# Kernel tuning notes

Hardware: AMD Instinct MI355X
Metric: run time of the kernel (lower is better)

## Reference

```python
import jax, jax.numpy as jnp
import numpy as np

B, H, W = 8, 512, 512
KSIZE = 11   # HVS Gaussian kernel size
SIGMA = 2.0
EPS = 1e-8


def _gauss_kernel():
    ax = jnp.arange(KSIZE, dtype=jnp.float32) - (KSIZE - 1) / 2.0
    g = jnp.exp(-(ax ** 2) / (2.0 * SIGMA ** 2))
    k = jnp.outer(g, g)
    return k / jnp.sum(k)


def _conv_same(x, k):
    # x: (B,1,H,W), k: (kh,kw) symmetric -> conv == correlation
    return jax.lax.conv_general_dilated(
        x, k[None, None, :, :], window_strides=(1, 1), padding='SAME',
        dimension_numbers=('NCHW', 'OIHW', 'NCHW'))


def setup_inputs() -> dict:
    key = jax.random.key(0)
    k1, k2, k3 = jax.random.split(key, 3)
    prob_map = jax.random.uniform(k1, (B, 1, H, W), dtype=jnp.float32,
                                  minval=0.01, maxval=0.99)
    c = jax.random.uniform(k2, (B, 1, H, W), dtype=jnp.float32)
    # binary halftone sampled per-pixel from prob_map
    h_sampled = (jax.random.uniform(k3, (B, 1, H, W)) < prob_map).astype(jnp.float32)
    return {"prob_map": prob_map, "c": c, "h_sampled": h_sampled}


def reference(prob_map, c, h_sampled):
    k = _gauss_kernel()
    # perceived error of the sampled halftone: e = G*h - c
    e = _conv_same(h_sampled, k) - c                     # (B,1,H,W)
    corr = _conv_same(e, k)                              # (G*e), G symmetric
    sum_k2 = jnp.sum(k * k)
    delta = 1.0 - 2.0 * h_sampled                        # flip change per pixel
    # reward_calc.compute_reward_with_flip, vectorized over all pixels:
    # E(flip at a) - E = 2*delta_a*(G*e)(a) + delta_a^2 * sum(G^2)
    reward = 2.0 * delta * corr + (delta ** 2) * sum_k2  # >0 means flip hurts
    log_prob = jnp.where(h_sampled > 0.5,
                         jnp.log(prob_map + EPS),
                         jnp.log(1.0 - prob_map + EPS))
    # local expected-gradient (REINFORCE) loss, averaged over batch
    loss = -jnp.sum(reward * log_prob) / prob_map.shape[0]
    return loss
```

## Files before the change

kernel.cpp:

```cpp
#include <hip/hip_runtime.h>

typedef float v2f __attribute__((ext_vector_type(2)));
typedef float v4f __attribute__((ext_vector_type(4)));

#define IMG 512
#define TS  32
#define TPB 2
#define NBLK 1024

#define A_STR  56
#define BT_STR 46
#define E_STR  44
#define CT_STR 34
#define C_STR  48

__device__ __forceinline__ v2f lo2(v4f v) { return __builtin_shufflevector(v, v, 0, 1); }
__device__ __forceinline__ v2f hi2(v4f v) { return __builtin_shufflevector(v, v, 2, 3); }

__device__ __forceinline__ v4f ldq(const float* __restrict__ hmap, size_t base,
                                   int x0, int y0, int idx) {
    int r = idx / 14, q = idx - r * 14;
    int gy = y0 - 10 + r, gx0 = x0 - 12 + 4 * q;
    v4f v = {0.f, 0.f, 0.f, 0.f};
    if ((unsigned)gy < IMG) {
        const float* hr = &hmap[base + ((size_t)gy << 9)];
        if (gx0 >= 0 && gx0 + 3 < IMG) {
            v = *(const v4f*)&hr[gx0];
        } else {
            if ((unsigned)(gx0 + 0) < IMG) v.x = hr[gx0 + 0];
            if ((unsigned)(gx0 + 1) < IMG) v.y = hr[gx0 + 1];
            if ((unsigned)(gx0 + 2) < IMG) v.z = hr[gx0 + 2];
            if ((unsigned)(gx0 + 3) < IMG) v.w = hr[gx0 + 3];
        }
    }
    return v;
}

__device__ __forceinline__ v4f ldc(const float* __restrict__ cmap, size_t base,
                                   int x0, int y0, int idx) {
    int r = idx / 12, q = idx - r * 12;
    int gy = y0 - 5 + r, gx0 = x0 - 8 + 4 * q;
    v4f v = {0.f, 0.f, 0.f, 0.f};
    if ((unsigned)gy < IMG) {
        const float* cr = &cmap[base + ((size_t)gy << 9)];
        if (gx0 >= 0 && gx0 + 3 < IMG) {
            v = *(const v4f*)&cr[gx0];
        } else {
            if ((unsigned)(gx0 + 0) < IMG) v.x = cr[gx0 + 0];
            if ((unsigned)(gx0 + 1) < IMG) v.y = cr[gx0 + 1];
            if ((unsigned)(gx0 + 2) < IMG) v.z = cr[gx0 + 2];
            if ((unsigned)(gx0 + 3) < IMG) v.w = cr[gx0 + 3];
        }
    }
    return v;
}

__global__ __launch_bounds__(256, 4) void marl_fused(
    const float* __restrict__ prob,
    const float* __restrict__ cmap,
    const float* __restrict__ hmap,
    float* __restrict__ out)
{
    __shared__ __align__(16) float Abuf[52 * A_STR];
    __shared__ __align__(16) float Bbuf[56 * BT_STR];
    __shared__ __align__(16) float Cbuf[42 * C_STR];
    __shared__ float red[4];

    const float W[11] = {0.00881223f, 0.02714358f, 0.06511405f, 0.12164908f,
                         0.17699840f, 0.20056540f, 0.17699840f, 0.12164908f,
                         0.06511405f, 0.02714358f, 0.00881223f};
    v2f wv[11];
#pragma unroll
    for (int i = 0; i < 11; ++i) wv[i] = (v2f){W[i], W[i]};
    float w2 = 0.f;
#pragma unroll
    for (int i = 0; i < 11; ++i) w2 += W[i] * W[i];
    const float sumk2 = w2 * w2;
    const v2f z = {0.f, 0.f};

    const int tid = threadIdx.x;
    const int wk  = (tid & 63) * 4 + (tid >> 6);
    const int i0 = tid, i1 = tid + 256, i2 = tid + 512;
    const int T0 = blockIdx.x * TPB;

    const int ox0 = 2 * (tid & 15), oy0e = 2 * (tid >> 4);

    v2f hv[TPB][2], pv[TPB][2];

    {
        const int b = T0 >> 8, r8 = T0 & 255;
        const int x0 = (r8 & 15) * TS, y0 = (r8 >> 4) * TS;
        const size_t base = (size_t)b << 18;
        v4f ha = ldq(hmap, base, x0, y0, i0);
        v4f hb = ldq(hmap, base, x0, y0, i1);
        v4f hc = (tid < 216) ? ldq(hmap, base, x0, y0, i2) : (v4f){0.f,0.f,0.f,0.f};
        v4f ca = ldc(cmap, base, x0, y0, i0);
        v4f cb = (tid < 248) ? ldc(cmap, base, x0, y0, i1) : (v4f){0.f,0.f,0.f,0.f};
#pragma unroll
        for (int h = 0; h < 2; ++h) {
            size_t rowb = base + ((size_t)(y0 + oy0e + h) << 9) + (x0 + ox0);
            hv[0][h] = *(const v2f*)&hmap[rowb];
            pv[0][h] = *(const v2f*)&prob[rowb];
        }
        { int r = i0 / 14, q = i0 - r * 14; *(v4f*)&Abuf[r * A_STR + 4 * q] = ha; }
        { int r = i1 / 14, q = i1 - r * 14; *(v4f*)&Abuf[r * A_STR + 4 * q] = hb; }
        if (tid < 216) { int r = i2 / 14, q = i2 - r * 14; *(v4f*)&Abuf[r * A_STR + 4 * q] = hc; }
        { int r = i0 / 12, q = i0 - r * 12; *(v4f*)&Cbuf[r * C_STR + 4 * q] = ca; }
        if (tid < 248) { int r = i1 / 12, q = i1 - r * 12; *(v4f*)&Cbuf[r * C_STR + 4 * q] = cb; }
    }
    __syncthreads();

    float partial = 0.f;
    v4f pfh0, pfh1, pfh2, pfc0, pfc1;

#pragma unroll
    for (int t = 0; t < TPB; ++t) {
        const int T = T0 + t;
        const int r8 = T & 255;
        const int x0 = (r8 & 15) * TS, y0 = (r8 >> 4) * TS;

        if (wk < 196) {
            int q = wk % 14, run = wk / 14;
            int by0 = 3 * run;
            v2f accLo[3] = {z, z, z}, accHi[3] = {z, z, z};
#pragma unroll
            for (int i = 0; i < 13; ++i) {
                v4f a = *(const v4f*)&Abuf[(by0 + i) * A_STR + 4 * q];
                v2f lo = lo2(a), hi = hi2(a);
#pragma unroll
                for (int r = 0; r < 3; ++r) {
                    int j = i - r;
                    if (j >= 0 && j < 11) { accLo[r] += wv[j] * lo; accHi[r] += wv[j] * hi; }
                }
            }
#pragma unroll
            for (int r = 0; r < 3; ++r) {
                int by = by0 + r;
                Bbuf[(4 * q + 0) * BT_STR + by] = accLo[r].x;
                Bbuf[(4 * q + 1) * BT_STR + by] = accLo[r].y;
                Bbuf[(4 * q + 2) * BT_STR + by] = accHi[r].x;
                Bbuf[(4 * q + 3) * BT_STR + by] = accHi[r].y;
            }
        }
        __syncthreads();

        if (wk < 231) {
            int eq = wk % 11, p = wk / 11;
            int ex0 = 4 * eq, ey0 = 2 * p;
            v2f acc[4] = {z, z, z, z};
#pragma unroll
            for (int i = 0; i < 14; ++i) {
                v2f bb = *(const v2f*)&Bbuf[(ex0 + 2 + i) * BT_STR + ey0];
#pragma unroll
                for (int c = 0; c < 4; ++c) {
                    int j = i - c;
                    if (j >= 0 && j < 11) acc[c] += wv[j] * bb;
                }
            }
#pragma unroll
            for (int c = 0; c < 4; ++c) {
                int ex = ex0 + c;
                if (ex < 42) {
                    int gx = x0 - 5 + ex;
                    bool xin = (unsigned)gx < IMG;
#pragma unroll
                    for (int h = 0; h < 2; ++h) {
                        int gy = y0 - 5 + ey0 + h;
                        float v = 0.f;
                        if (xin && (unsigned)gy < IMG)
                            v = acc[c][h] - Cbuf[(ey0 + h) * C_STR + ex + 3];
                        Abuf[(ey0 + h) * E_STR + ex] = v;
                    }
                }
            }
        }
        __syncthreads();

        if (t + 1 < TPB) {
            const int Tn = T + 1;
            const int nb = Tn >> 8, nr8 = Tn & 255;
            const int nx0 = (nr8 & 15) * TS, ny0 = (nr8 >> 4) * TS;
            const size_t nbase = (size_t)nb << 18;
            pfh0 = ldq(hmap, nbase, nx0, ny0, i0);
            pfh1 = ldq(hmap, nbase, nx0, ny0, i1);
            if (tid < 216) pfh2 = ldq(hmap, nbase, nx0, ny0, i2);
            pfc0 = ldc(cmap, nbase, nx0, ny0, i0);
            if (tid < 248) pfc1 = ldc(cmap, nbase, nx0, ny0, i1);
#pragma unroll
            for (int h = 0; h < 2; ++h) {
                size_t rowb = nbase + ((size_t)(ny0 + oy0e + h) << 9) + (nx0 + ox0);
                hv[t + 1][h] = *(const v2f*)&hmap[rowb];
                pv[t + 1][h] = *(const v2f*)&prob[rowb];
            }
        }
        if (wk < 176) {
            int eq = wk % 11, run = wk / 11;
            int ex0 = 4 * eq, oyb = 2 * run;
            v2f accLo[2] = {z, z}, accHi[2] = {z, z};
#pragma unroll
            for (int i = 0; i < 12; ++i) {
                v4f e = *(const v4f*)&Abuf[(oyb + i) * E_STR + ex0];
                v2f lo = lo2(e), hi = hi2(e);
#pragma unroll
                for (int r = 0; r < 2; ++r) {
                    int j = i - r;
                    if (j >= 0 && j < 11) { accLo[r] += wv[j] * lo; accHi[r] += wv[j] * hi; }
                }
            }
#pragma unroll
            for (int r = 0; r < 2; ++r) {
                int oy = oyb + r;
                Bbuf[(ex0 + 0) * CT_STR + oy] = accLo[r].x;
                Bbuf[(ex0 + 1) * CT_STR + oy] = accLo[r].y;
                if (ex0 + 2 < 42) {
                    Bbuf[(ex0 + 2) * CT_STR + oy] = accHi[r].x;
                    Bbuf[(ex0 + 3) * CT_STR + oy] = accHi[r].y;
                }
            }
        }
        __syncthreads();

        if (t + 1 < TPB) {
            { int r = i0 / 14, q = i0 - r * 14; *(v4f*)&Abuf[r * A_STR + 4 * q] = pfh0; }
            { int r = i1 / 14, q = i1 - r * 14; *(v4f*)&Abuf[r * A_STR + 4 * q] = pfh1; }
            if (tid < 216) { int r = i2 / 14, q = i2 - r * 14; *(v4f*)&Abuf[r * A_STR + 4 * q] = pfh2; }
            { int r = i0 / 12, q = i0 - r * 12; *(v4f*)&Cbuf[r * C_STR + 4 * q] = pfc0; }
            if (tid < 248) { int r = i1 / 12, q = i1 - r * 12; *(v4f*)&Cbuf[r * C_STR + 4 * q] = pfc1; }
        }
        {
            v2f acc[2] = {z, z};
#pragma unroll
            for (int i = 0; i < 12; ++i) {
                v2f ct = *(const v2f*)&Bbuf[(ox0 + i) * CT_STR + oy0e];
#pragma unroll
                for (int c = 0; c < 2; ++c) {
                    int j = i - c;
                    if (j >= 0 && j < 11) acc[c] += wv[j] * ct;
                }
            }
#pragma unroll
            for (int h = 0; h < 2; ++h) {
#pragma unroll
                for (int c = 0; c < 2; ++c) {
                    float h_ = hv[t][h][c], p_ = pv[t][h][c];
                    float logp = __logf(h_ > 0.5f ? p_ + 1e-8f : 1.f - p_ + 1e-8f);
                    float delta = 1.f - 2.f * h_;
                    partial += (2.f * delta * acc[c][h] + sumk2) * logp;
                }
            }
        }
        __syncthreads();
    }

#pragma unroll
    for (int off = 32; off > 0; off >>= 1)
        partial += __shfl_down(partial, off, 64);
    if ((tid & 63) == 0) red[tid >> 6] = partial;
    __syncthreads();
    if (tid == 0) {
        float s = red[0] + red[1] + red[2] + red[3];
        atomicAdd(out, s * -0.125f);
    }
}

extern "C" void kernel_launch(void* const* d_in, const int* in_sizes, int n_in,
                              void* d_out, int out_size, void* d_ws, size_t ws_size,
                              hipStream_t stream) {
    const float* prob = (const float*)d_in[0];
    const float* cmap = (const float*)d_in[1];
    const float* hmap = (const float*)d_in[2];
    float* out = (float*)d_out;

    hipMemsetAsync(out, 0, sizeof(float), stream);

    marl_fused<<<dim3(NBLK), dim3(256), 0, stream>>>(prob, cmap, hmap, out);
}
```

Measured before the change: 94.71 us.

## Use 32x16 tiles, one tile per block, and swizzle the error buffer in LDS

Replaces the two-tiles-per-block 32x32 scheme (with register prefetch of the next tile) by one 32x16 tile per block over 4096 blocks. Halo loads, work mappings and LDS strides are reworked to fit the smaller tile, and the error buffer gets an XOR swizzle to cut LDS bank conflicts. Launch bounds rise to 8 blocks per CU to raise occupancy. The cost is more halo overhead per output pixel, since the halo ratio is worse for shorter tiles, plus more idle threads in each stage and the loss of the cross-tile prefetch overlap.

```diff
diff --git a/kernel.cpp b/kernel.cpp
--- a/kernel.cpp
+++ b/kernel.cpp
@@ -4,15 +4,15 @@
 typedef float v4f __attribute__((ext_vector_type(4)));
 
 #define IMG 512
-#define TS  32
-#define TPB 2
-#define NBLK 1024
-
-#define A_STR  56
-#define BT_STR 46
-#define E_STR  44
-#define CT_STR 34
-#define C_STR  48
+#define TSX 32
+#define TSY 16
+#define NBLK 4096
+
+#define A_STR  60
+#define BT_STR 28
+#define E_STR  64
+#define CT_STR 18
+#define C_STR  49
 
 __device__ __forceinline__ v2f lo2(v4f v) { return __builtin_shufflevector(v, v, 0, 1); }
 __device__ __forceinline__ v2f hi2(v4f v) { return __builtin_shufflevector(v, v, 2, 3); }
@@ -55,15 +55,15 @@
     return v;
 }
 
-__global__ __launch_bounds__(256, 4) void marl_fused(
+__global__ __launch_bounds__(256, 8) void marl_fused(
     const float* __restrict__ prob,
     const float* __restrict__ cmap,
     const float* __restrict__ hmap,
     float* __restrict__ out)
 {
-    __shared__ __align__(16) float Abuf[52 * A_STR];
+    __shared__ __align__(16) float Abuf[36 * A_STR];
     __shared__ __align__(16) float Bbuf[56 * BT_STR];
-    __shared__ __align__(16) float Cbuf[42 * C_STR];
+    __shared__ __align__(16) float Cbuf[26 * C_STR];
     __shared__ float red[4];
 
     const float W[11] = {0.00881223f, 0.02714358f, 0.06511405f, 0.12164908f,
@@ -79,177 +79,148 @@
     const v2f z = {0.f, 0.f};
 
     const int tid = threadIdx.x;
-    const int wk  = (tid & 63) * 4 + (tid >> 6);
-    const int i0 = tid, i1 = tid + 256, i2 = tid + 512;
-    const int T0 = blockIdx.x * TPB;
-
-    const int ox0 = 2 * (tid & 15), oy0e = 2 * (tid >> 4);
-
-    v2f hv[TPB][2], pv[TPB][2];
-
+    const int T  = blockIdx.x;
+    const int b  = T >> 9, r9 = T & 511;
+    const int x0 = (r9 & 15) * TSX, y0 = (r9 >> 4) * TSY;
+    const size_t base = (size_t)b << 18;
+
+    const int ox0 = 2 * (tid >> 3), oy0e = 2 * (tid & 7);
+
+    v2f hv[2], pv[2];
     {
-        const int b = T0 >> 8, r8 = T0 & 255;
-        const int x0 = (r8 & 15) * TS, y0 = (r8 >> 4) * TS;
-        const size_t base = (size_t)b << 18;
-        v4f ha = ldq(hmap, base, x0, y0, i0);
-        v4f hb = ldq(hmap, base, x0, y0, i1);
-        v4f hc = (tid < 216) ? ldq(hmap, base, x0, y0, i2) : (v4f){0.f,0.f,0.f,0.f};
-        v4f ca = ldc(cmap, base, x0, y0, i0);
-        v4f cb = (tid < 248) ? ldc(cmap, base, x0, y0, i1) : (v4f){0.f,0.f,0.f,0.f};
-#pragma unroll
-        for (int h = 0; h < 2; ++h) {
-            size_t rowb = base + ((size_t)(y0 + oy0e + h) << 9) + (x0 + ox0);
-            hv[0][h] = *(const v2f*)&hmap[rowb];
-            pv[0][h] = *(const v2f*)&prob[rowb];
-        }
-        { int r = i0 / 14, q = i0 - r * 14; *(v4f*)&Abuf[r * A_STR + 4 * q] = ha; }
-        { int r = i1 / 14, q = i1 - r * 14; *(v4f*)&Abuf[r * A_STR + 4 * q] = hb; }
-        if (tid < 216) { int r = i2 / 14, q = i2 - r * 14; *(v4f*)&Abuf[r * A_STR + 4 * q] = hc; }
-        { int r = i0 / 12, q = i0 - r * 12; *(v4f*)&Cbuf[r * C_STR + 4 * q] = ca; }
-        if (tid < 248) { int r = i1 / 12, q = i1 - r * 12; *(v4f*)&Cbuf[r * C_STR + 4 * q] = cb; }
-    }
-    __syncthreads();
-
-    float partial = 0.f;
-    v4f pfh0, pfh1, pfh2, pfc0, pfc1;
-
-#pragma unroll
-    for (int t = 0; t < TPB; ++t) {
-        const int T = T0 + t;
-        const int r8 = T & 255;
-        const int x0 = (r8 & 15) * TS, y0 = (r8 >> 4) * TS;
-
-        if (wk < 196) {
-            int q = wk % 14, run = wk / 14;
-            int by0 = 3 * run;
-            v2f accLo[3] = {z, z, z}, accHi[3] = {z, z, z};
-#pragma unroll
-            for (int i = 0; i < 13; ++i) {
-                v4f a = *(const v4f*)&Abuf[(by0 + i) * A_STR + 4 * q];
-                v2f lo = lo2(a), hi = hi2(a);
-#pragma unroll
-                for (int r = 0; r < 3; ++r) {
-                    int j = i - r;
-                    if (j >= 0 && j < 11) { accLo[r] += wv[j] * lo; accHi[r] += wv[j] * hi; }
-                }
-            }
+        v4f ha = ldq(hmap, base, x0, y0, tid);
+        v4f hb = (tid < 248) ? ldq(hmap, base, x0, y0, tid + 256) : (v4f){0.f,0.f,0.f,0.f};
+        v4f ca = ldc(cmap, base, x0, y0, tid);
+        v4f cb = (tid < 56) ? ldc(cmap, base, x0, y0, tid + 256) : (v4f){0.f,0.f,0.f,0.f};
+        if (tid < 128) {
+#pragma unroll
+            for (int h = 0; h < 2; ++h) {
+                size_t rowb = base + ((size_t)(y0 + oy0e + h) << 9) + (x0 + ox0);
+                hv[h] = *(const v2f*)&hmap[rowb];
+                pv[h] = *(const v2f*)&prob[rowb];
+            }
+        }
+        { int r = tid / 14, q = tid - r * 14; *(v4f*)&Abuf[r * A_STR + 4 * q] = ha; }
+        if (tid < 248) { int i = tid + 256, r = i / 14, q = i - r * 14;
+                         *(v4f*)&Abuf[r * A_STR + 4 * q] = hb; }
+        { int r = tid / 12, q = tid - r * 12; float* d = &Cbuf[r * C_STR + 4 * q];
+          d[0] = ca.x; d[1] = ca.y; d[2] = ca.z; d[3] = ca.w; }
+        if (tid < 56) { int i = tid + 256, r = i / 12, q = i - r * 12;
+                        float* d = &Cbuf[r * C_STR + 4 * q];
+                        d[0] = cb.x; d[1] = cb.y; d[2] = cb.z; d[3] = cb.w; }
+    }
+    __syncthreads();
+
+    if (tid < 126) {
+        int q = tid / 9, run = tid - 9 * q;
+        int by0 = 3 * run;
+        v2f accLo[3] = {z, z, z}, accHi[3] = {z, z, z};
+#pragma unroll
+        for (int i = 0; i < 13; ++i) {
+            v4f a = *(const v4f*)&Abuf[(by0 + i) * A_STR + 4 * q];
+            v2f lo = lo2(a), hi = hi2(a);
 #pragma unroll
             for (int r = 0; r < 3; ++r) {
-                int by = by0 + r;
+                int j = i - r;
+                if (j >= 0 && j < 11) { accLo[r] += wv[j] * lo; accHi[r] += wv[j] * hi; }
+            }
+        }
+#pragma unroll
+        for (int r = 0; r < 3; ++r) {
+            int by = by0 + r;
+            if (by < 26) {
                 Bbuf[(4 * q + 0) * BT_STR + by] = accLo[r].x;
                 Bbuf[(4 * q + 1) * BT_STR + by] = accLo[r].y;
                 Bbuf[(4 * q + 2) * BT_STR + by] = accHi[r].x;
                 Bbuf[(4 * q + 3) * BT_STR + by] = accHi[r].y;
             }
         }
-        __syncthreads();
-
-        if (wk < 231) {
-            int eq = wk % 11, p = wk / 11;
-            int ex0 = 4 * eq, ey0 = 2 * p;
-            v2f acc[4] = {z, z, z, z};
-#pragma unroll
-            for (int i = 0; i < 14; ++i) {
-                v2f bb = *(const v2f*)&Bbuf[(ex0 + 2 + i) * BT_STR + ey0];
-#pragma unroll
-                for (int c = 0; c < 4; ++c) {
-                    int j = i - c;
-                    if (j >= 0 && j < 11) acc[c] += wv[j] * bb;
+    }
+    __syncthreads();
+
+    if (tid < 143) {
+        int eq = tid / 13, p = tid - 13 * eq;
+        int ex0 = 4 * eq, ey0 = 2 * p;
+        v2f acc[4] = {z, z, z, z};
+#pragma unroll
+        for (int i = 0; i < 14; ++i) {
+            v2f bb = *(const v2f*)&Bbuf[(ex0 + 2 + i) * BT_STR + ey0];
+#pragma unroll
+            for (int c = 0; c < 4; ++c) {
+                int j = i - c;
+                if (j >= 0 && j < 11) acc[c] += wv[j] * bb;
+            }
+        }
+        int swz = (p & 7) << 2;
+#pragma unroll
+        for (int c = 0; c < 4; ++c) {
+            int ex = ex0 + c;
+            if (ex < 42) {
+                int gx = x0 - 5 + ex;
+                bool xin = (unsigned)gx < IMG;
+#pragma unroll
+                for (int h = 0; h < 2; ++h) {
+                    int gy = y0 - 5 + ey0 + h;
+                    float v = 0.f;
+                    if (xin && (unsigned)gy < IMG)
+                        v = acc[c][h] - Cbuf[(ey0 + h) * C_STR + ex + 3];
+                    Abuf[(ey0 + h) * E_STR + (ex ^ swz)] = v;
                 }
             }
-#pragma unroll
-            for (int c = 0; c < 4; ++c) {
-                int ex = ex0 + c;
-                if (ex < 42) {
-                    int gx = x0 - 5 + ex;
-                    bool xin = (unsigned)gx < IMG;
-#pragma unroll
-                    for (int h = 0; h < 2; ++h) {
-                        int gy = y0 - 5 + ey0 + h;
-                        float v = 0.f;
-                        if (xin && (unsigned)gy < IMG)
-                            v = acc[c][h] - Cbuf[(ey0 + h) * C_STR + ex + 3];
-                        Abuf[(ey0 + h) * E_STR + ex] = v;
-                    }
-                }
-            }
-        }
-        __syncthreads();
-
-        if (t + 1 < TPB) {
-            const int Tn = T + 1;
-            const int nb = Tn >> 8, nr8 = Tn & 255;
-            const int nx0 = (nr8 & 15) * TS, ny0 = (nr8 >> 4) * TS;
-            const size_t nbase = (size_t)nb << 18;
-            pfh0 = ldq(hmap, nbase, nx0, ny0, i0);
-            pfh1 = ldq(hmap, nbase, nx0, ny0, i1);
-            if (tid < 216) pfh2 = ldq(hmap, nbase, nx0, ny0, i2);
-            pfc0 = ldc(cmap, nbase, nx0, ny0, i0);
-            if (tid < 248) pfc1 = ldc(cmap, nbase, nx0, ny0, i1);
-#pragma unroll
-            for (int h = 0; h < 2; ++h) {
-                size_t rowb = nbase + ((size_t)(ny0 + oy0e + h) << 9) + (nx0 + ox0);
-                hv[t + 1][h] = *(const v2f*)&hmap[rowb];
-                pv[t + 1][h] = *(const v2f*)&prob[rowb];
-            }
-        }
-        if (wk < 176) {
-            int eq = wk % 11, run = wk / 11;
-            int ex0 = 4 * eq, oyb = 2 * run;
-            v2f accLo[2] = {z, z}, accHi[2] = {z, z};
-#pragma unroll
-            for (int i = 0; i < 12; ++i) {
-                v4f e = *(const v4f*)&Abuf[(oyb + i) * E_STR + ex0];
-                v2f lo = lo2(e), hi = hi2(e);
-#pragma unroll
-                for (int r = 0; r < 2; ++r) {
-                    int j = i - r;
-                    if (j >= 0 && j < 11) { accLo[r] += wv[j] * lo; accHi[r] += wv[j] * hi; }
-                }
-            }
+        }
+    }
+    __syncthreads();
+
+    if (tid < 88) {
+        int eq = tid >> 3, run = tid & 7;
+        int ex0 = 4 * eq, oy0 = 2 * run;
+        v2f accLo[2] = {z, z}, accHi[2] = {z, z};
+#pragma unroll
+        for (int i = 0; i < 12; ++i) {
+            int row = oy0 + i;
+            v4f e = *(const v4f*)&Abuf[row * E_STR + (ex0 ^ (((row >> 1) & 7) << 2))];
+            v2f lo = lo2(e), hi = hi2(e);
 #pragma unroll
             for (int r = 0; r < 2; ++r) {
-                int oy = oyb + r;
-                Bbuf[(ex0 + 0) * CT_STR + oy] = accLo[r].x;
-                Bbuf[(ex0 + 1) * CT_STR + oy] = accLo[r].y;
-                if (ex0 + 2 < 42) {
-                    Bbuf[(ex0 + 2) * CT_STR + oy] = accHi[r].x;
-                    Bbuf[(ex0 + 3) * CT_STR + oy] = accHi[r].y;
-                }
-            }
-        }
-        __syncthreads();
-
-        if (t + 1 < TPB) {
-            { int r = i0 / 14, q = i0 - r * 14; *(v4f*)&Abuf[r * A_STR + 4 * q] = pfh0; }
-            { int r = i1 / 14, q = i1 - r * 14; *(v4f*)&Abuf[r * A_STR + 4 * q] = pfh1; }
-            if (tid < 216) { int r = i2 / 14, q = i2 - r * 14; *(v4f*)&Abuf[r * A_STR + 4 * q] = pfh2; }
-            { int r = i0 / 12, q = i0 - r * 12; *(v4f*)&Cbuf[r * C_STR + 4 * q] = pfc0; }
-            if (tid < 248) { int r = i1 / 12, q = i1 - r * 12; *(v4f*)&Cbuf[r * C_STR + 4 * q] = pfc1; }
-        }
-        {
-            v2f acc[2] = {z, z};
-#pragma unroll
-            for (int i = 0; i < 12; ++i) {
-                v2f ct = *(const v2f*)&Bbuf[(ox0 + i) * CT_STR + oy0e];
-#pragma unroll
-                for (int c = 0; c < 2; ++c) {
-                    int j = i - c;
-                    if (j >= 0 && j < 11) acc[c] += wv[j] * ct;
-                }
-            }
-#pragma unroll
-            for (int h = 0; h < 2; ++h) {
-#pragma unroll
-                for (int c = 0; c < 2; ++c) {
-                    float h_ = hv[t][h][c], p_ = pv[t][h][c];
-                    float logp = __logf(h_ > 0.5f ? p_ + 1e-8f : 1.f - p_ + 1e-8f);
-                    float delta = 1.f - 2.f * h_;
-                    partial += (2.f * delta * acc[c][h] + sumk2) * logp;
-                }
-            }
-        }
-        __syncthreads();
+                int j = i - r;
+                if (j >= 0 && j < 11) { accLo[r] += wv[j] * lo; accHi[r] += wv[j] * hi; }
+            }
+        }
+#pragma unroll
+        for (int r = 0; r < 2; ++r) {
+            int oy = oy0 + r;
+            Bbuf[(ex0 + 0) * CT_STR + oy] = accLo[r].x;
+            Bbuf[(ex0 + 1) * CT_STR + oy] = accLo[r].y;
+            if (ex0 + 2 < 42) {
+                Bbuf[(ex0 + 2) * CT_STR + oy] = accHi[r].x;
+                Bbuf[(ex0 + 3) * CT_STR + oy] = accHi[r].y;
+            }
+        }
+    }
+    __syncthreads();
+
+    float partial = 0.f;
+    if (tid < 128) {
+        v2f acc[2] = {z, z};
+#pragma unroll
+        for (int i = 0; i < 12; ++i) {
+            v2f ct = *(const v2f*)&Bbuf[(ox0 + i) * CT_STR + oy0e];
+#pragma unroll
+            for (int c = 0; c < 2; ++c) {
+                int j = i - c;
+                if (j >= 0 && j < 11) acc[c] += wv[j] * ct;
+            }
+        }
+#pragma unroll
+        for (int h = 0; h < 2; ++h) {
+#pragma unroll
+            for (int c = 0; c < 2; ++c) {
+                float h_ = hv[h][c], p_ = pv[h][c];
+                float logp = __logf(h_ > 0.5f ? p_ + 1e-8f : 1.f - p_ + 1e-8f);
+                float delta = 1.f - 2.f * h_;
+                partial += (2.f * delta * acc[c][h] + sumk2) * logp;
+            }
+        }
     }
 
 #pragma unroll
```

After: 134.6 us. +42.1%, slower.

## Keep c in registers, transpose e buffer, remap thread work per conv pass

Applied to the files above, without the earlier changes.

Removes the shared-memory staging of the target image c and instead loads each thread's needed c values directly into registers with scalar global loads, freeing LDS. The intermediate error tile e is now stored transposed so the second vertical pass reads contiguous vectors per thread and computes 8 outputs from a 20-wide register window. Thread-to-work mappings are changed: the first vertical pass uses fewer threads each computing 6 rows, and the final pass swaps x/y roles. It trades more per-thread register use and uncoalesced scalar c loads for lower LDS footprint and fewer LDS reads.

```diff
diff --git a/kernel.cpp b/kernel.cpp
--- a/kernel.cpp
+++ b/kernel.cpp
@@ -8,11 +8,10 @@
 #define TPB 2
 #define NBLK 1024
 
-#define A_STR  56
+#define A_STR  58
 #define BT_STR 46
-#define E_STR  44
-#define CT_STR 34
-#define C_STR  48
+#define ET_STR 44
+#define CT_STR 36
 
 __device__ __forceinline__ v2f lo2(v4f v) { return __builtin_shufflevector(v, v, 0, 1); }
 __device__ __forceinline__ v2f hi2(v4f v) { return __builtin_shufflevector(v, v, 2, 3); }
@@ -36,25 +35,6 @@
     return v;
 }
 
-__device__ __forceinline__ v4f ldc(const float* __restrict__ cmap, size_t base,
-                                   int x0, int y0, int idx) {
-    int r = idx / 12, q = idx - r * 12;
-    int gy = y0 - 5 + r, gx0 = x0 - 8 + 4 * q;
-    v4f v = {0.f, 0.f, 0.f, 0.f};
-    if ((unsigned)gy < IMG) {
-        const float* cr = &cmap[base + ((size_t)gy << 9)];
-        if (gx0 >= 0 && gx0 + 3 < IMG) {
-            v = *(const v4f*)&cr[gx0];
-        } else {
-            if ((unsigned)(gx0 + 0) < IMG) v.x = cr[gx0 + 0];
-            if ((unsigned)(gx0 + 1) < IMG) v.y = cr[gx0 + 1];
-            if ((unsigned)(gx0 + 2) < IMG) v.z = cr[gx0 + 2];
-            if ((unsigned)(gx0 + 3) < IMG) v.w = cr[gx0 + 3];
-        }
-    }
-    return v;
-}
-
 __global__ __launch_bounds__(256, 4) void marl_fused(
     const float* __restrict__ prob,
     const float* __restrict__ cmap,
@@ -63,7 +43,6 @@
 {
     __shared__ __align__(16) float Abuf[52 * A_STR];
     __shared__ __align__(16) float Bbuf[56 * BT_STR];
-    __shared__ __align__(16) float Cbuf[42 * C_STR];
     __shared__ float red[4];
 
     const float W[11] = {0.00881223f, 0.02714358f, 0.06511405f, 0.12164908f,
@@ -79,13 +58,16 @@
     const v2f z = {0.f, 0.f};
 
     const int tid = threadIdx.x;
-    const int wk  = (tid & 63) * 4 + (tid >> 6);
     const int i0 = tid, i1 = tid + 256, i2 = tid + 512;
     const int T0 = blockIdx.x * TPB;
 
-    const int ox0 = 2 * (tid & 15), oy0e = 2 * (tid >> 4);
+    const int p1run = tid % 7, p1q = tid / 7;
+    const int p2p = tid % 21, p2eq = tid / 21;
+    const int p3oyq = tid & 3, p3ex = tid >> 2;
+    const int oy0e = 2 * (tid & 15), ox0 = 2 * (tid >> 4);
 
     v2f hv[TPB][2], pv[TPB][2];
+    float creg[TPB][2][4];
 
     {
         const int b = T0 >> 8, r8 = T0 & 255;
@@ -94,8 +76,18 @@
         v4f ha = ldq(hmap, base, x0, y0, i0);
         v4f hb = ldq(hmap, base, x0, y0, i1);
         v4f hc = (tid < 216) ? ldq(hmap, base, x0, y0, i2) : (v4f){0.f,0.f,0.f,0.f};
-        v4f ca = ldc(cmap, base, x0, y0, i0);
-        v4f cb = (tid < 248) ? ldc(cmap, base, x0, y0, i1) : (v4f){0.f,0.f,0.f,0.f};
+        if (tid < 231) {
+#pragma unroll
+            for (int h = 0; h < 2; ++h) {
+                int gy = y0 - 5 + 2 * p2p + h;
+#pragma unroll
+                for (int c = 0; c < 4; ++c) {
+                    int gx = x0 - 5 + 4 * p2eq + c;
+                    creg[0][h][c] = ((unsigned)gy < IMG && (unsigned)gx < IMG)
+                        ? cmap[base + ((size_t)gy << 9) + gx] : 0.f;
+                }
+            }
+        }
 #pragma unroll
         for (int h = 0; h < 2; ++h) {
             size_t rowb = base + ((size_t)(y0 + oy0e + h) << 9) + (x0 + ox0);
@@ -105,13 +97,11 @@
         { int r = i0 / 14, q = i0 - r * 14; *(v4f*)&Abuf[r * A_STR + 4 * q] = ha; }
         { int r = i1 / 14, q = i1 - r * 14; *(v4f*)&Abuf[r * A_STR + 4 * q] = hb; }
         if (tid < 216) { int r = i2 / 14, q = i2 - r * 14; *(v4f*)&Abuf[r * A_STR + 4 * q] = hc; }
-        { int r = i0 / 12, q = i0 - r * 12; *(v4f*)&Cbuf[r * C_STR + 4 * q] = ca; }
-        if (tid < 248) { int r = i1 / 12, q = i1 - r * 12; *(v4f*)&Cbuf[r * C_STR + 4 * q] = cb; }
     }
     __syncthreads();
 
     float partial = 0.f;
-    v4f pfh0, pfh1, pfh2, pfc0, pfc1;
+    v4f pfh0, pfh1, pfh2;
 
 #pragma unroll
     for (int t = 0; t < TPB; ++t) {
@@ -119,34 +109,32 @@
         const int r8 = T & 255;
         const int x0 = (r8 & 15) * TS, y0 = (r8 >> 4) * TS;
 
-        if (wk < 196) {
-            int q = wk % 14, run = wk / 14;
-            int by0 = 3 * run;
-            v2f accLo[3] = {z, z, z}, accHi[3] = {z, z, z};
-#pragma unroll
-            for (int i = 0; i < 13; ++i) {
-                v4f a = *(const v4f*)&Abuf[(by0 + i) * A_STR + 4 * q];
+        if (tid < 98) {
+            int by0 = 6 * p1run;
+            v2f accLo[6] = {z, z, z, z, z, z}, accHi[6] = {z, z, z, z, z, z};
+#pragma unroll
+            for (int i = 0; i < 16; ++i) {
+                v4f a = *(const v4f*)&Abuf[(by0 + i) * A_STR + 4 * p1q];
                 v2f lo = lo2(a), hi = hi2(a);
 #pragma unroll
-                for (int r = 0; r < 3; ++r) {
+                for (int r = 0; r < 6; ++r) {
                     int j = i - r;
                     if (j >= 0 && j < 11) { accLo[r] += wv[j] * lo; accHi[r] += wv[j] * hi; }
                 }
             }
 #pragma unroll
-            for (int r = 0; r < 3; ++r) {
+            for (int r = 0; r < 6; ++r) {
                 int by = by0 + r;
-                Bbuf[(4 * q + 0) * BT_STR + by] = accLo[r].x;
-                Bbuf[(4 * q + 1) * BT_STR + by] = accLo[r].y;
-                Bbuf[(4 * q + 2) * BT_STR + by] = accHi[r].x;
-                Bbuf[(4 * q + 3) * BT_STR + by] = accHi[r].y;
-            }
-        }
-        __syncthreads();
-
-        if (wk < 231) {
-            int eq = wk % 11, p = wk / 11;
-            int ex0 = 4 * eq, ey0 = 2 * p;
+                Bbuf[(4 * p1q + 0) * BT_STR + by] = accLo[r].x;
+                Bbuf[(4 * p1q + 1) * BT_STR + by] = accLo[r].y;
+                Bbuf[(4 * p1q + 2) * BT_STR + by] = accHi[r].x;
+                Bbuf[(4 * p1q + 3) * BT_STR + by] = accHi[r].y;
+            }
+        }
+        __syncthreads();
+
+        if (tid < 231) {
+            int ex0 = 4 * p2eq, ey0 = 2 * p2p;
             v2f acc[4] = {z, z, z, z};
 #pragma unroll
             for (int i = 0; i < 14; ++i) {
@@ -168,8 +156,8 @@
                         int gy = y0 - 5 + ey0 + h;
                         float v = 0.f;
                         if (xin && (unsigned)gy < IMG)
-                            v = acc[c][h] - Cbuf[(ey0 + h) * C_STR + ex + 3];
-                        Abuf[(ey0 + h) * E_STR + ex] = v;
+                            v = acc[c][h] - creg[t][h][c];
+                        Abuf[ex * ET_STR + ey0 + h] = v;
                     }
                 }
             }
@@ -184,8 +172,18 @@
             pfh0 = ldq(hmap, nbase, nx0, ny0, i0);
             pfh1 = ldq(hmap, nbase, nx0, ny0, i1);
             if (tid < 216) pfh2 = ldq(hmap, nbase, nx0, ny0, i2);
-            pfc0 = ldc(cmap, nbase, nx0, ny0, i0);
-            if (tid < 248) pfc1 = ldc(cmap, nbase, nx0, ny0, i1);
+            if (tid < 231) {
+#pragma unroll
+                for (int h = 0; h < 2; ++h) {
+                    int gy = ny0 - 5 + 2 * p2p + h;
+#pragma unroll
+                    for (int c = 0; c < 4; ++c) {
+                        int gx = nx0 - 5 + 4 * p2eq + c;
+                        creg[t + 1][h][c] = ((unsigned)gy < IMG && (unsigned)gx < IMG)
+                            ? cmap[nbase + ((size_t)gy << 9) + gx] : 0.f;
+                    }
+                }
+            }
 #pragma unroll
             for (int h = 0; h < 2; ++h) {
                 size_t rowb = nbase + ((size_t)(ny0 + oy0e + h) << 9) + (nx0 + ox0);
@@ -193,30 +191,27 @@
                 pv[t + 1][h] = *(const v2f*)&prob[rowb];
             }
         }
-        if (wk < 176) {
-            int eq = wk % 11, run = wk / 11;
-            int ex0 = 4 * eq, oyb = 2 * run;
-            v2f accLo[2] = {z, z}, accHi[2] = {z, z};
-#pragma unroll
-            for (int i = 0; i < 12; ++i) {
-                v4f e = *(const v4f*)&Abuf[(oyb + i) * E_STR + ex0];
-                v2f lo = lo2(e), hi = hi2(e);
-#pragma unroll
-                for (int r = 0; r < 2; ++r) {
-                    int j = i - r;
-                    if (j >= 0 && j < 11) { accLo[r] += wv[j] * lo; accHi[r] += wv[j] * hi; }
-                }
-            }
-#pragma unroll
-            for (int r = 0; r < 2; ++r) {
-                int oy = oyb + r;
-                Bbuf[(ex0 + 0) * CT_STR + oy] = accLo[r].x;
-                Bbuf[(ex0 + 1) * CT_STR + oy] = accLo[r].y;
-                if (ex0 + 2 < 42) {
-                    Bbuf[(ex0 + 2) * CT_STR + oy] = accHi[r].x;
-                    Bbuf[(ex0 + 3) * CT_STR + oy] = accHi[r].y;
-                }
-            }
+        if (tid < 168) {
+            int oy0 = 8 * p3oyq;
+            const float* src = &Abuf[p3ex * ET_STR + oy0];
+            v4f w0 = *(const v4f*)&src[0];
+            v4f w1 = *(const v4f*)&src[4];
+            v4f w2_ = *(const v4f*)&src[8];
+            v4f w3 = *(const v4f*)&src[12];
+            v4f w4 = *(const v4f*)&src[16];
+            float win[20];
+            *(v4f*)&win[0] = w0; *(v4f*)&win[4] = w1; *(v4f*)&win[8] = w2_;
+            *(v4f*)&win[12] = w3; *(v4f*)&win[16] = w4;
+            float o[8];
+#pragma unroll
+            for (int k = 0; k < 8; ++k) {
+                float acc = 0.f;
+#pragma unroll
+                for (int j = 0; j < 11; ++j) acc += W[j] * win[k + j];
+                o[k] = acc;
+            }
+            *(v4f*)&Bbuf[p3ex * CT_STR + oy0]     = (v4f){o[0], o[1], o[2], o[3]};
+            *(v4f*)&Bbuf[p3ex * CT_STR + oy0 + 4] = (v4f){o[4], o[5], o[6], o[7]};
         }
         __syncthreads();
 
@@ -224,8 +219,6 @@
             { int r = i0 / 14, q = i0 - r * 14; *(v4f*)&Abuf[r * A_STR + 4 * q] = pfh0; }
             { int r = i1 / 14, q = i1 - r * 14; *(v4f*)&Abuf[r * A_STR + 4 * q] = pfh1; }
             if (tid < 216) { int r = i2 / 14, q = i2 - r * 14; *(v4f*)&Abuf[r * A_STR + 4 * q] = pfh2; }
-            { int r = i0 / 12, q = i0 - r * 12; *(v4f*)&Cbuf[r * C_STR + 4 * q] = pfc0; }
-            if (tid < 248) { int r = i1 / 12, q = i1 - r * 12; *(v4f*)&Cbuf[r * C_STR + 4 * q] = pfc1; }
         }
         {
             v2f acc[2] = {z, z};
```

Result: faster. 91.07 us (-3.9%).
